# Kernel tuning notes

Hardware: AMD Instinct MI355X
Metric: run time of the kernel (lower is better)

The kernel has to match this reference:

```python
import jax, jax.numpy as jnp
import numpy as np

B, S, D, H = 1, 2048, 1024, 16
DEPTH = D // H          # 64
A_DFF = 1024
NRES = 2                # num_reslayerA
SLOPE = 0.2             # LeakyReLU slope in plga attention
POW_EPS = 1e-9


def _ln(x, g, b):
    m = jnp.mean(x, axis=-1, keepdims=True)
    v = jnp.var(x, axis=-1, keepdims=True)
    return (x - m) * jax.lax.rsqrt(v + 1e-6) * g + b


def setup_inputs() -> dict:
    key = jax.random.key(0)
    ks = jax.random.split(key, 12)
    s = 0.02
    W = lambda k, shp: jax.random.normal(k, shp, jnp.float32) * s
    return {
        'q': jax.random.normal(ks[0], (B, S, D), jnp.float32),
        'k': jax.random.normal(ks[1], (B, S, D), jnp.float32),
        'v': jax.random.normal(ks[2], (B, S, D), jnp.float32),
        'mask': jnp.zeros((B, 1, 1, S), jnp.float32),
        'wq_w': W(ks[3], (D, D)), 'wq_b': jnp.zeros((D,), jnp.float32),
        'wk_w': W(ks[4], (D, D)), 'wk_b': jnp.zeros((D,), jnp.float32),
        'wv_w': W(ks[5], (D, D)), 'wv_b': jnp.zeros((D,), jnp.float32),
        'wo_w': W(ks[6], (D, D)), 'wo_b': jnp.zeros((D,), jnp.float32),
        # stacked ResLayerA params: Dense(depth->A_dff, relu) -> Dense(A_dff->depth) -> LN
        'rl_w1': W(ks[7], (NRES, DEPTH, A_DFF)), 'rl_b1': jnp.zeros((NRES, A_DFF), jnp.float32),
        'rl_w2': W(ks[8], (NRES, A_DFF, DEPTH)), 'rl_b2': jnp.zeros((NRES, DEPTH), jnp.float32),
        'rl_g': jnp.ones((NRES, DEPTH), jnp.float32), 'rl_beta': jnp.zeros((NRES, DEPTH), jnp.float32),
        # plga layer params: power coefficients, attention vector, bias
        'pw': jnp.ones((DEPTH,), jnp.float32),
        'a_vec': W(ks[9], (DEPTH,)),
        'ba': jnp.zeros((), jnp.float32),
    }


def reference(q, k, v, mask, wq_w, wq_b, wk_w, wk_b, wv_w, wv_b, wo_w, wo_b,
              rl_w1, rl_b1, rl_w2, rl_b2, rl_g, rl_beta, pw, a_vec, ba):
    Bq = q.shape[0]
    split = lambda x: x.reshape(Bq, -1, H, DEPTH).transpose(0, 2, 1, 3)  # [b,h,s,d]
    qh = split(q @ wq_w + wq_b)
    kh = split(k @ wk_w + wk_b)
    vh = split(v @ wv_w + wv_b)

    # metric tensor A = q^T q  -> [b,h,depth,depth]
    A = jnp.einsum('bhsd,bhse->bhde', qh, qh)
    # ResLayerA residual dense+LN stack over last dim
    for i in range(NRES):
        Ain = A
        hdn = jax.nn.relu(A @ rl_w1[i] + rl_b1[i])
        A = _ln((hdn @ rl_w2[i] + rl_b2[i]) + Ain, rl_g[i], rl_beta[i])

    # power-law graph attention (plga_layer, att_head=1, activation=None)
    Ap = jnp.power(jnp.abs(A) + POW_EPS, pw)                  # element-wise learned power
    avAp = jnp.einsum('d,bhde->bhe', a_vec, Ap)               # [b,h,depth] per-dim scaling
    E = jnp.einsum('bhsd,bhd,bhtd->bhst', qh, avAp, kh)       # pairwise logits [b,h,s,s]
    Ep = jnp.where(E > 0, E, SLOPE * E) + ba                  # LeakyReLU + learned bias
    Ep = Ep + mask * (-1e9)
    attv = jax.nn.softmax(Ep, axis=-1)
    Hnext = jnp.einsum('bhst,bhtd->bhsd', attv, vh)

    Hnext = Hnext.transpose(0, 2, 1, 3).reshape(Bq, -1, D)
    out = Hnext @ wo_w + wo_b
    return (out, E, A, pw, attv, ba, avAp, Ep)
```

## Files before the change

kernel.cpp:

```cpp
#include <hip/hip_runtime.h>
#include <stdint.h>

#define S_ 2048
#define D_ 1024
#define H_ 16
#define DEP_ 64

typedef float f32x4 __attribute__((ext_vector_type(4)));
typedef __bf16 bf16x8 __attribute__((ext_vector_type(8)));

#define MFMA16(a,b,c) __builtin_amdgcn_mfma_f32_16x16x32_bf16((a),(b),(c),0,0,0)

static constexpr size_t OFF_E    = 2097152ull;
static constexpr size_t OFF_A    = 69206016ull;
static constexpr size_t OFF_PW   = 69271552ull;
static constexpr size_t OFF_ATT  = 69271616ull;
static constexpr size_t OFF_BA   = 136380480ull;
static constexpr size_t OFF_AVAP = 136380481ull;
static constexpr size_t OFF_EP   = 136381505ull;

__device__ __forceinline__ short f2b(float f) {
  union { float f; uint32_t u; } c; c.f = f;
  uint32_t u = c.u;
  uint32_t r = (u + 0x7fffu + ((u >> 16) & 1u)) >> 16;
  return (short)(r & 0xffffu);
}
__device__ __forceinline__ float b2f(short s) {
  union { uint32_t u; float f; } c; c.u = ((uint32_t)(uint16_t)s) << 16;
  return c.f;
}
__device__ __forceinline__ void st_nt(float* p, f32x4 v) {
  __builtin_nontemporal_store(v, (f32x4*)p);
}

__global__ void k_cvt_in(const float* __restrict__ q, const float* __restrict__ k,
                         const float* __restrict__ v, short* __restrict__ dst) {
  const float* src = (blockIdx.z == 0) ? q : (blockIdx.z == 1) ? k : v;
  short* d = dst + (size_t)blockIdx.z * (S_*D_);
  int i = (blockIdx.x * 256 + threadIdx.x) * 4;
  float4 f = *(const float4*)(src + i);
  short4 o;
  o.x = f2b(f.x); o.y = f2b(f.y); o.z = f2b(f.z); o.w = f2b(f.w);
  *(short4*)(d + i) = o;
}

__global__ void k_cvt_wT(const float* __restrict__ wq, const float* __restrict__ wk,
                         const float* __restrict__ wv, const float* __restrict__ wo,
                         short* __restrict__ dst) {
  __shared__ float tile[64][65];
  const float* W = (blockIdx.z == 0) ? wq : (blockIdx.z == 1) ? wk :
                   (blockIdx.z == 2) ? wv : wo;
  short* d = dst + (size_t)blockIdx.z * (D_*D_);
  int k0 = blockIdx.x * 64, n0 = blockIdx.y * 64;
  int t = threadIdx.x;
  for (int i = 0; i < 16; ++i) {
    int e = i*256 + t, r = e >> 6, c = e & 63;
    tile[r][c] = W[(size_t)(k0+r)*D_ + n0 + c];
  }
  __syncthreads();
  for (int i = 0; i < 16; ++i) {
    int e = i*256 + t, r = e >> 6, c = e & 63;
    d[(size_t)(n0+r)*D_ + k0 + c] = f2b(tile[c][r]);
  }
}

__global__ void k_cvt_rl(const float* __restrict__ w1, const float* __restrict__ w2,
                         short* __restrict__ w1T, short* __restrict__ w2T) {
  __shared__ float tile[64][65];
  int z = blockIdx.z, l = z >> 1, which = z & 1;
  int bx = blockIdx.x, t = threadIdx.x;
  if (which == 0) {
    const float* src = w1 + (size_t)l*65536;
    short* d = w1T + (size_t)l*65536;
    int n0 = bx*64;
    for (int i = 0; i < 16; ++i) {
      int e = i*256 + t, r = e >> 6, c = e & 63;
      tile[r][c] = src[(size_t)r*1024 + n0 + c];
    }
    __syncthreads();
    for (int i = 0; i < 16; ++i) {
      int e = i*256 + t, r = e >> 6, c = e & 63;
      d[(size_t)(n0+r)*64 + c] = f2b(tile[c][r]);
    }
  } else {
    const float* src = w2 + (size_t)l*65536;
    short* d = w2T + (size_t)l*65536;
    int k0 = bx*64;
    for (int i = 0; i < 16; ++i) {
      int e = i*256 + t, r = e >> 6, c = e & 63;
      tile[r][c] = src[(size_t)(k0+r)*64 + c];
    }
    __syncthreads();
    for (int i = 0; i < 16; ++i) {
      int e = i*256 + t, r = e >> 6, c = e & 63;
      d[(size_t)r*1024 + k0 + c] = f2b(tile[c][r]);
    }
  }
}

__global__ __launch_bounds__(256) void k_gemm(
    const short* __restrict__ Xall, const short* __restrict__ X2,
    const short* __restrict__ WTall,
    const float* __restrict__ b0, const float* __restrict__ b1v,
    const float* __restrict__ b2v, short* __restrict__ dstall,
    float* __restrict__ outf, int mode) {
  __shared__ short As[128*72];
  __shared__ short Bs[128*72];
  int z = blockIdx.z;
  const short* X  = Xall + (size_t)z * (S_*D_);
  const short* WT = WTall + (size_t)z * (D_*D_);
  int m0 = blockIdx.x * 128, n0 = blockIdx.y * 128;
  int t = threadIdx.x, lane = t & 63;
  int wr = t >> 7, wc = (t >> 6) & 1;
  int rA = lane & 15, kg = lane >> 4;
  f32x4 acc[4][4] = {};
  for (int kt = 0; kt < 16; ++kt) {
#pragma unroll
    for (int i = 0; i < 4; ++i) {
      int cid = i*256 + t, row = cid >> 3, c = cid & 7;
      size_t xi = (size_t)(m0+row)*D_ + kt*64 + c*8;
      if (mode == 2) {
        union { int4 v; short s[8]; } a1, a2, o;
        a1.v = *(const int4*)&X[xi];
        a2.v = *(const int4*)&X2[xi];
#pragma unroll
        for (int j = 0; j < 8; ++j) o.s[j] = f2b(b2f(a1.s[j]) + b2f(a2.s[j]));
        *(int4*)&As[row*72 + c*8] = o.v;
      } else {
        *(int4*)&As[row*72 + c*8] = *(const int4*)&X[xi];
      }
      *(int4*)&Bs[row*72 + c*8] = *(const int4*)&WT[(size_t)(n0+row)*D_ + kt*64 + c*8];
    }
    __syncthreads();
#pragma unroll
    for (int kk = 0; kk < 2; ++kk) {
      bf16x8 a[4], b[4];
#pragma unroll
      for (int m = 0; m < 4; ++m)
        a[m] = *(const bf16x8*)&As[(wr*64 + m*16 + rA)*72 + kk*32 + kg*8];
#pragma unroll
      for (int n = 0; n < 4; ++n)
        b[n] = *(const bf16x8*)&Bs[(wc*64 + n*16 + rA)*72 + kk*32 + kg*8];
#pragma unroll
      for (int m = 0; m < 4; ++m)
#pragma unroll
        for (int n = 0; n < 4; ++n)
          acc[m][n] = MFMA16(a[m], b[n], acc[m][n]);
    }
    __syncthreads();
  }
  const float* bias = (mode != 0) ? b0 : (z == 0 ? b0 : (z == 1 ? b1v : b2v));
#pragma unroll
  for (int m = 0; m < 4; ++m) {
#pragma unroll
    for (int n = 0; n < 4; ++n) {
      int col = n0 + wc*64 + n*16 + rA;
      float bb = bias[col];
#pragma unroll
      for (int rr = 0; rr < 4; ++rr) {
        int row = m0 + wr*64 + m*16 + kg*4 + rr;
        float val = acc[m][n][rr] + bb;
        if (mode == 0) {
          int head = col >> 6, dd = col & 63;
          dstall[(size_t)z*(S_*D_) + ((size_t)head*S_ + row)*DEP_ + dd] = f2b(val);
        } else {
          outf[(size_t)row*D_ + col] = val;
        }
      }
    }
  }
}

__global__ void k_transpose(const short* __restrict__ qh, const short* __restrict__ vh,
                            short* __restrict__ qhT, short* __restrict__ vhT) {
  __shared__ short tile[64][68];
  const short* src = blockIdx.z ? vh : qh;
  short* dst = blockIdx.z ? vhT : qhT;
  int h = blockIdx.y, s0 = blockIdx.x * 64, t = threadIdx.x;
  for (int i = 0; i < 16; ++i) {
    int e = i*256 + t, r = e >> 6, c = e & 63;
    tile[r][c] = src[((size_t)h*S_ + s0 + r)*DEP_ + c];
  }
  __syncthreads();
  for (int i = 0; i < 16; ++i) {
    int e = i*256 + t, r = e >> 6, c = e & 63;
    dst[((size_t)h*DEP_ + r)*S_ + s0 + c] = tile[c][r];
  }
}

__global__ __launch_bounds__(256) void k_metric_p(const short* __restrict__ qhT,
                                                  float* __restrict__ Apart) {
  __shared__ short qt[64*72];
  int kc = blockIdx.x, h = blockIdx.y, t = threadIdx.x, lane = t & 63;
  int wr = t >> 7, wc = (t >> 6) & 1;
  int rA = lane & 15, kg = lane >> 4;
  f32x4 acc[2][2] = {};
  for (int kt = 0; kt < 4; ++kt) {
#pragma unroll
    for (int i = 0; i < 2; ++i) {
      int cid = i*256 + t, row = cid >> 3, c = cid & 7;
      *(int4*)&qt[row*72 + c*8] =
        *(const int4*)&qhT[((size_t)h*DEP_ + row)*S_ + kc*256 + kt*64 + c*8];
    }
    __syncthreads();
#pragma unroll
    for (int kk = 0; kk < 2; ++kk) {
      bf16x8 a[2], b[2];
#pragma unroll
      for (int m = 0; m < 2; ++m)
        a[m] = *(const bf16x8*)&qt[(wr*32 + m*16 + rA)*72 + kk*32 + kg*8];
#pragma unroll
      for (int n = 0; n < 2; ++n)
        b[n] = *(const bf16x8*)&qt[(wc*32 + n*16 + rA)*72 + kk*32 + kg*8];
#pragma unroll
      for (int m = 0; m < 2; ++m)
#pragma unroll
        for (int n = 0; n < 2; ++n)
          acc[m][n] = MFMA16(a[m], b[n], acc[m][n]);
    }
    __syncthreads();
  }
#pragma unroll
  for (int m = 0; m < 2; ++m)
#pragma unroll
    for (int n = 0; n < 2; ++n)
#pragma unroll
      for (int rr = 0; rr < 4; ++rr) {
        int row = wr*32 + m*16 + kg*4 + rr, col = wc*32 + n*16 + rA;
        Apart[((size_t)(kc*16 + h))*4096 + row*64 + col] = acc[m][n][rr];
      }
}

__global__ void k_metric_r(const float* __restrict__ Apart, float* __restrict__ A0f,
                           short* __restrict__ Afb) {
  int h = blockIdx.x, t = threadIdx.x;
#pragma unroll
  for (int i = 0; i < 4; ++i) {
    int idx = i*1024 + t*4;
    f32x4 s = {};
#pragma unroll
    for (int kc = 0; kc < 8; ++kc)
      s += *(const f32x4*)&Apart[((size_t)(kc*16 + h))*4096 + idx];
    *(f32x4*)&A0f[(size_t)h*4096 + idx] = s;
    union { int2 v; short sh[4]; } pk;
#pragma unroll
    for (int j = 0; j < 4; ++j) pk.sh[j] = f2b(s[j]);
    *(int2*)&Afb[(size_t)h*4096 + idx] = pk.v;
  }
}

__global__ __launch_bounds__(256) void k_d1(const short* __restrict__ Afb,
                                            const short* __restrict__ w1Tl,
                                            const float* __restrict__ b1l,
                                            short* __restrict__ hd) {
  __shared__ short As[64*72];
  __shared__ short Bs[128*72];
  int bcol = blockIdx.x * 128, h = blockIdx.y;
  int t = threadIdx.x, lane = t & 63, w = t >> 6;
  int rA = lane & 15, kg = lane >> 4;
#pragma unroll
  for (int i = 0; i < 2; ++i) {
    int cid = i*256 + t, row = cid >> 3, c = cid & 7;
    *(int4*)&As[row*72 + c*8] = *(const int4*)&Afb[(size_t)h*4096 + row*64 + c*8];
  }
#pragma unroll
  for (int i = 0; i < 4; ++i) {
    int cid = i*256 + t, row = cid >> 3, c = cid & 7;
    *(int4*)&Bs[row*72 + c*8] = *(const int4*)&w1Tl[(size_t)(bcol+row)*64 + c*8];
  }
  __syncthreads();
  f32x4 acc[2][4] = {};
#pragma unroll
  for (int kk = 0; kk < 2; ++kk) {
    bf16x8 aA[4], bW[2];
#pragma unroll
    for (int mf = 0; mf < 4; ++mf)
      aA[mf] = *(const bf16x8*)&As[(mf*16 + rA)*72 + kk*32 + kg*8];
#pragma unroll
    for (int nf = 0; nf < 2; ++nf)
      bW[nf] = *(const bf16x8*)&Bs[(w*32 + nf*16 + rA)*72 + kk*32 + kg*8];
#pragma unroll
    for (int nf = 0; nf < 2; ++nf)
#pragma unroll
      for (int mf = 0; mf < 4; ++mf)
        acc[nf][mf] = MFMA16(bW[nf], aA[mf], acc[nf][mf]);
  }
#pragma unroll
  for (int nf = 0; nf < 2; ++nf) {
    int cb = bcol + w*32 + nf*16 + kg*4;
    f32x4 b1v = *(const f32x4*)&b1l[cb];
#pragma unroll
    for (int mf = 0; mf < 4; ++mf) {
      int r = mf*16 + rA;
      union { int2 v; short s[4]; } pk;
#pragma unroll
      for (int rr = 0; rr < 4; ++rr)
        pk.s[rr] = f2b(fmaxf(acc[nf][mf][rr] + b1v[rr], 0.f));
      *(int2*)&hd[((size_t)h*64 + r)*1024 + cb] = pk.v;
    }
  }
}

__global__ __launch_bounds__(256) void k_d2p(const short* __restrict__ hd,
                                             const short* __restrict__ w2Tl,
                                             float* __restrict__ d2part) {
  __shared__ short hs[64*72];
  __shared__ short ws2[64*72];
  int kc = blockIdx.x, h = blockIdx.y, t = threadIdx.x, lane = t & 63;
  int wr = t >> 7, wc = (t >> 6) & 1;
  int rA = lane & 15, kg = lane >> 4;
  f32x4 acc[2][2] = {};
  for (int kt = 0; kt < 4; ++kt) {
#pragma unroll
    for (int i = 0; i < 2; ++i) {
      int cid = i*256 + t, row = cid >> 3, c = cid & 7;
      *(int4*)&hs[row*72 + c*8]  =
        *(const int4*)&hd[((size_t)h*64 + row)*1024 + kc*256 + kt*64 + c*8];
      *(int4*)&ws2[row*72 + c*8] =
        *(const int4*)&w2Tl[(size_t)row*1024 + kc*256 + kt*64 + c*8];
    }
    __syncthreads();
#pragma unroll
    for (int kk = 0; kk < 2; ++kk) {
      bf16x8 a[2], b[2];
#pragma unroll
      for (int m = 0; m < 2; ++m)
        a[m] = *(const bf16x8*)&hs[(wr*32 + m*16 + rA)*72 + kk*32 + kg*8];
#pragma unroll
      for (int n = 0; n < 2; ++n)
        b[n] = *(const bf16x8*)&ws2[(wc*32 + n*16 + rA)*72 + kk*32 + kg*8];
#pragma unroll
      for (int m = 0; m < 2; ++m)
#pragma unroll
        for (int n = 0; n < 2; ++n)
          acc[m][n] = MFMA16(a[m], b[n], acc[m][n]);
    }
    __syncthreads();
  }
#pragma unroll
  for (int m = 0; m < 2; ++m)
#pragma unroll
    for (int n = 0; n < 2; ++n)
#pragma unroll
      for (int rr = 0; rr < 4; ++rr) {
        int row = wr*32 + m*16 + kg*4 + rr, col = wc*32 + n*16 + rA;
        d2part[((size_t)(kc*16 + h))*4096 + row*64 + col] = acc[m][n][rr];
      }
}

__global__ __launch_bounds__(256) void k_d2r_ln(
    const float* __restrict__ d2part, const float* __restrict__ b2l,
    const float* __restrict__ AresIn, const float* __restrict__ gl,
    const float* __restrict__ bel, short* __restrict__ Afb,
    float* __restrict__ AresOut, float* __restrict__ outB,
    const float* __restrict__ pwv, const float* __restrict__ av,
    const float* __restrict__ bav, float* __restrict__ avApW, int layer) {
  __shared__ float Xf[64][68];
  __shared__ float red[4][64];
  int h = blockIdx.x, t = threadIdx.x;
  int r = t >> 2, q4 = t & 3;
  float xv[16], s1 = 0.f, s2 = 0.f;
#pragma unroll
  for (int jj = 0; jj < 4; ++jj) {
    f32x4 s = {};
#pragma unroll
    for (int kc = 0; kc < 4; ++kc)
      s += *(const f32x4*)&d2part[((size_t)(kc*16 + h))*4096 + r*64 + q4*16 + jj*4];
#pragma unroll
    for (int j = 0; j < 4; ++j) {
      int c = q4*16 + jj*4 + j;
      float x = s[j] + b2l[c] + AresIn[(size_t)h*4096 + r*64 + c];
      xv[jj*4 + j] = x;
      s1 += x; s2 += x*x;
    }
  }
  s1 += __shfl_xor(s1, 1); s1 += __shfl_xor(s1, 2);
  s2 += __shfl_xor(s2, 1); s2 += __shfl_xor(s2, 2);
  float mean = s1 * (1.f/64.f);
  float var  = s2 * (1.f/64.f) - mean*mean;
  float rstd = rsqrtf(var + 1e-6f);
#pragma unroll
  for (int j = 0; j < 16; ++j) {
    int c = q4*16 + j;
    float nx = (xv[j] - mean)*rstd*gl[c] + bel[c];
    Afb[(size_t)h*4096 + r*64 + c] = f2b(nx);
    if (layer == 0) AresOut[(size_t)h*4096 + r*64 + c] = nx;
    else            outB[OFF_A + (size_t)h*4096 + r*64 + c] = nx;
    Xf[r][c] = nx;
  }
  if (layer == 1) {
    __syncthreads();
    int e = t & 63, dg = t >> 6;
    float pe = pwv[e], p = 0.f;
    for (int j = 0; j < 16; ++j) {
      int d = dg*16 + j;
      p += av[d] * powf(fabsf(Xf[d][e]) + 1e-9f, pe);
    }
    red[dg][e] = p;
    __syncthreads();
    if (t < 64) {
      float tot = red[0][t] + red[1][t] + red[2][t] + red[3][t];
      avApW[h*64 + t] = tot;
      outB[OFF_AVAP + h*64 + t] = tot;
    }
    if (h == 0) {
      if (t < 64) outB[OFF_PW + t] = pwv[t];
      if (t == 0) outB[OFF_BA] = bav[0];
    }
  }
}

__global__ __launch_bounds__(256) void k_pass1(
    const short* __restrict__ qh, const short* __restrict__ kh,
    const float* __restrict__ avAp, const float* __restrict__ mask,
    const float* __restrict__ bap, float* __restrict__ outB,
    float2* __restrict__ part) {
  __shared__ float Et[128*128];
  __shared__ float avl[64];
  short* Qs = (short*)Et;
  short* Ks = ((short*)Et) + 8192;
  int tt = blockIdx.x, st = blockIdx.y, h = blockIdx.z;
  int s0 = st*128, t0 = tt*128;
  int t = threadIdx.x, lane = t & 63;
  int wr = t >> 7, wc = (t >> 6) & 1;
  int rA = lane & 15, kg = lane >> 4;
  if (t < 16) *(f32x4*)&avl[t*4] = *(const f32x4*)&avAp[h*64 + t*4];
  __syncthreads();
#pragma unroll
  for (int i = 0; i < 4; ++i) {
    int cid = i*256 + t, row = cid >> 3, c = cid & 7, cs = c ^ (row & 7);
    union { int4 v; short s[8]; } qa, qo;
    qa.v = *(const int4*)&qh[((size_t)h*S_ + s0 + row)*DEP_ + c*8];
#pragma unroll
    for (int j = 0; j < 8; ++j) qo.s[j] = f2b(b2f(qa.s[j]) * avl[c*8 + j]);
    *(int4*)&Qs[row*64 + cs*8] = qo.v;
    *(int4*)&Ks[row*64 + cs*8] = *(const int4*)&kh[((size_t)h*S_ + t0 + row)*DEP_ + c*8];
  }
  __syncthreads();
  f32x4 acc[4][4] = {};
#pragma unroll
  for (int kk = 0; kk < 2; ++kk) {
    bf16x8 a[4], b[4];
#pragma unroll
    for (int m = 0; m < 4; ++m) {
      int row = wr*64 + m*16 + rA, c = (kk*4 + kg) ^ (row & 7);
      a[m] = *(const bf16x8*)&Qs[row*64 + c*8];
    }
#pragma unroll
    for (int n = 0; n < 4; ++n) {
      int row = wc*64 + n*16 + rA, c = (kk*4 + kg) ^ (row & 7);
      b[n] = *(const bf16x8*)&Ks[row*64 + c*8];
    }
#pragma unroll
    for (int m = 0; m < 4; ++m)
#pragma unroll
      for (int n = 0; n < 4; ++n)
        acc[m][n] = MFMA16(b[n], a[m], acc[m][n]);
  }
  float bav = bap[0];
  f32x4 mk[4];
#pragma unroll
  for (int n = 0; n < 4; ++n) {
    f32x4 mm = *(const f32x4*)&mask[t0 + wc*64 + n*16 + kg*4];
#pragma unroll
    for (int j = 0; j < 4; ++j) mk[n][j] = mm[j] * (-1e9f);
  }
#pragma unroll
  for (int m = 0; m < 4; ++m) {
    int row = s0 + wr*64 + m*16 + rA;
    float mx = -3.4e38f;
    f32x4 ep4[4];
#pragma unroll
    for (int n = 0; n < 4; ++n) {
      f32x4 e = acc[m][n];
      f32x4 ep;
#pragma unroll
      for (int j = 0; j < 4; ++j) {
        float ee = e[j];
        ep[j] = (ee > 0.f ? ee : 0.2f*ee) + bav + mk[n][j];
        mx = fmaxf(mx, ep[j]);
      }
      ep4[n] = ep;
    }
    mx = fmaxf(mx, __shfl_xor(mx, 16));
    mx = fmaxf(mx, __shfl_xor(mx, 32));
    float sm = 0.f;
#pragma unroll
    for (int n = 0; n < 4; ++n)
#pragma unroll
      for (int j = 0; j < 4; ++j) sm += expf(ep4[n][j] - mx);
    sm += __shfl_xor(sm, 16);
    sm += __shfl_xor(sm, 32);
    if (kg == 0)
      part[((size_t)(h*S_ + row)*16 + tt)*2 + wc] = make_float2(mx, sm);
  }
  __syncthreads();
#pragma unroll
  for (int m = 0; m < 4; ++m)
#pragma unroll
    for (int n = 0; n < 4; ++n) {
      int row = wr*64 + m*16 + rA;
      int unit = wc*16 + n*4 + kg;
      *(f32x4*)&Et[row*128 + ((unit ^ (row & 7)))*4] = acc[m][n];
    }
  __syncthreads();
  float* Eo  = outB + OFF_E;
  float* Epo = outB + OFF_EP;
  int colu = t & 31;
  int rbase = t >> 5;
  f32x4 mm4 = *(const f32x4*)&mask[t0 + colu*4];
  f32x4 mk4;
#pragma unroll
  for (int j = 0; j < 4; ++j) mk4[j] = mm4[j] * (-1e9f);
#pragma unroll
  for (int r = 0; r < 16; ++r) {
    int row = r*8 + rbase;
    f32x4 e = *(const f32x4*)&Et[row*128 + ((colu ^ (row & 7)))*4];
    size_t gb = ((size_t)h*S_ + s0 + row)*S_ + t0 + colu*4;
    st_nt(&Eo[gb], e);
    f32x4 ep;
#pragma unroll
    for (int j = 0; j < 4; ++j)
      ep[j] = (e[j] > 0.f ? e[j] : 0.2f*e[j]) + bav + mk4[j];
    st_nt(&Epo[gb], ep);
  }
}

__global__ void k_sreduce(const float2* __restrict__ part, float2* __restrict__ fin) {
  int row = blockIdx.x * 256 + threadIdx.x;
  const float2* pp = part + (size_t)row * 32;
  float M = -3.4e38f;
  float2 p[32];
#pragma unroll
  for (int i = 0; i < 32; ++i) { p[i] = pp[i]; M = fmaxf(M, p[i].x); }
  float L = 0.f;
#pragma unroll
  for (int i = 0; i < 32; ++i) L += p[i].y * expf(p[i].x - M);
  fin[row] = make_float2(M, L);
}

__global__ __launch_bounds__(256) void k_pass2(
    const short* __restrict__ qh, const short* __restrict__ kh,
    const short* __restrict__ vhT, const float* __restrict__ avAp,
    const float* __restrict__ mask, const float* __restrict__ bap,
    const float2* __restrict__ fin, float* __restrict__ attv,
    short* __restrict__ Hnp) {
  __shared__ short Qs[128*64];
  __shared__ short KP[128*128];
  __shared__ short Vs[64*128];
  __shared__ float avl[64];
  int st = blockIdx.x, tc = blockIdx.y, h = blockIdx.z;
  int s0 = st * 128;
  int t = threadIdx.x, lane = t & 63;
  int wr = t >> 7, wc = (t >> 6) & 1;
  int rA = lane & 15, kg = lane >> 4;
  if (t < 16) *(f32x4*)&avl[t*4] = *(const f32x4*)&avAp[h*64 + t*4];
  __syncthreads();
#pragma unroll
  for (int i = 0; i < 4; ++i) {
    int cid = i*256 + t, row = cid >> 3, c = cid & 7, cs = c ^ (row & 7);
    union { int4 v; short s[8]; } qa, qo;
    qa.v = *(const int4*)&qh[((size_t)h*S_ + s0 + row)*DEP_ + c*8];
#pragma unroll
    for (int j = 0; j < 8; ++j) qo.s[j] = f2b(b2f(qa.s[j]) * avl[c*8 + j]);
    *(int4*)&Qs[row*64 + cs*8] = qo.v;
  }
  float Ms[4], Li[4];
#pragma unroll
  for (int m = 0; m < 4; ++m) {
    float2 f = fin[h*S_ + s0 + wr*64 + m*16 + rA];
    Ms[m] = f.x; Li[m] = 1.f / f.y;
  }
  float bav = bap[0];
  __syncthreads();
  bf16x8 aq[4][2];
#pragma unroll
  for (int m = 0; m < 4; ++m)
#pragma unroll
    for (int kk = 0; kk < 2; ++kk) {
      int row = wr*64 + m*16 + rA, c = (kk*4 + kg) ^ (row & 7);
      aq[m][kk] = *(const bf16x8*)&Qs[row*64 + c*8];
    }
  f32x4 acc2[4][2] = {};
  for (int tt = tc*8; tt < tc*8 + 8; ++tt) {
    int t0 = tt * 128;
    __syncthreads();
#pragma unroll
    for (int i = 0; i < 4; ++i) {
      int cid = i*256 + t, row = cid >> 3, c = cid & 7, cs = c ^ (row & 7);
      *(int4*)&KP[row*64 + cs*8] = *(const int4*)&kh[((size_t)h*S_ + t0 + row)*DEP_ + c*8];
    }
#pragma unroll
    for (int i = 0; i < 4; ++i) {
      int cid = i*256 + t, row = cid >> 4, c = cid & 15, cs = c ^ (row & 7);
      *(int4*)&Vs[row*128 + cs*8] = *(const int4*)&vhT[((size_t)h*DEP_ + row)*S_ + t0 + c*8];
    }
    __syncthreads();
    f32x4 accE[4][4] = {};
#pragma unroll
    for (int kk = 0; kk < 2; ++kk) {
      bf16x8 b[4];
#pragma unroll
      for (int n = 0; n < 4; ++n) {
        int row = wc*64 + n*16 + rA, c = (kk*4 + kg) ^ (row & 7);
        b[n] = *(const bf16x8*)&KP[row*64 + c*8];
      }
#pragma unroll
      for (int m = 0; m < 4; ++m)
#pragma unroll
        for (int n = 0; n < 4; ++n)
          accE[m][n] = MFMA16(b[n], aq[m][kk], accE[m][n]);
    }
    f32x4 mk[4];
#pragma unroll
    for (int n = 0; n < 4; ++n) {
      f32x4 mm = *(const f32x4*)&mask[t0 + wc*64 + n*16 + kg*4];
#pragma unroll
      for (int j = 0; j < 4; ++j) mk[n][j] = mm[j] * (-1e9f);
    }
#pragma unroll
    for (int m = 0; m < 4; ++m)
#pragma unroll
      for (int n = 0; n < 4; ++n) {
        f32x4 e = accE[m][n], p;
#pragma unroll
        for (int j = 0; j < 4; ++j) {
          float ep = (e[j] > 0.f ? e[j] : 0.2f*e[j]) + bav + mk[n][j];
          p[j] = expf(ep - Ms[m]) * Li[m];
        }
        accE[m][n] = p;
      }
    __syncthreads();
#pragma unroll
    for (int m = 0; m < 4; ++m) {
      int srow = wr*64 + m*16 + rA;
#pragma unroll
      for (int n = 0; n < 4; ++n) {
        int tcol = wc*64 + n*16 + kg*4;
        union { int2 v; short s[4]; } pk;
#pragma unroll
        for (int j = 0; j < 4; ++j) pk.s[j] = f2b(accE[m][n][j]);
        *(int2*)((char*)KP + srow*256 + ((tcol*2) ^ ((srow & 7) << 4))) = pk.v;
      }
    }
    __syncthreads();
#pragma unroll
    for (int kkp = 0; kkp < 4; ++kkp) {
      bf16x8 ap[4], bv[2];
#pragma unroll
      for (int m = 0; m < 4; ++m) {
        int row = wr*64 + m*16 + rA;
        ap[m] = *(const bf16x8*)((const char*)KP + row*256 + ((kkp*64 + kg*16) ^ ((row & 7) << 4)));
      }
#pragma unroll
      for (int n = 0; n < 2; ++n) {
        int dd = wc*32 + n*16 + rA, c = (kkp*4 + kg) ^ (dd & 7);
        bv[n] = *(const bf16x8*)&Vs[dd*128 + c*8];
      }
#pragma unroll
      for (int m = 0; m < 4; ++m)
#pragma unroll
        for (int n = 0; n < 2; ++n)
          acc2[m][n] = MFMA16(ap[m], bv[n], acc2[m][n]);
    }
#pragma unroll
    for (int it = 0; it < 8; ++it) {
      int row = it*16 + (t >> 4);
      int unit = t & 15;
      union { int4 v; short s[8]; } pv;
      pv.v = *(const int4*)((const char*)KP + row*256 + ((unit*16) ^ ((row & 7) << 4)));
      f32x4 lo, hi;
#pragma unroll
      for (int j = 0; j < 4; ++j) { lo[j] = b2f(pv.s[j]); hi[j] = b2f(pv.s[4+j]); }
      size_t gb = ((size_t)h*S_ + s0 + row)*S_ + t0 + unit*8;
      st_nt(&attv[gb], lo);
      st_nt(&attv[gb + 4], hi);
    }
  }
  short* Hp = Hnp + (size_t)tc * (S_*D_);
#pragma unroll
  for (int m = 0; m < 4; ++m)
#pragma unroll
    for (int n = 0; n < 2; ++n)
#pragma unroll
      for (int rr = 0; rr < 4; ++rr) {
        int row = s0 + wr*64 + m*16 + kg*4 + rr;
        int dd = wc*32 + n*16 + rA;
        Hp[(size_t)row*D_ + h*DEP_ + dd] = f2b(acc2[m][n][rr]);
      }
}

extern "C" void kernel_launch(void* const* d_in, const int* in_sizes, int n_in,
                              void* d_out, int out_size, void* d_ws, size_t ws_size,
                              hipStream_t stream) {
  (void)in_sizes; (void)n_in; (void)out_size; (void)ws_size;
  const float* q    = (const float*)d_in[0];
  const float* k    = (const float*)d_in[1];
  const float* v    = (const float*)d_in[2];
  const float* mask = (const float*)d_in[3];
  const float* wq_w = (const float*)d_in[4];
  const float* wq_b = (const float*)d_in[5];
  const float* wk_w = (const float*)d_in[6];
  const float* wk_b = (const float*)d_in[7];
  const float* wv_w = (const float*)d_in[8];
  const float* wv_b = (const float*)d_in[9];
  const float* wo_w = (const float*)d_in[10];
  const float* wo_b = (const float*)d_in[11];
  const float* rl_w1 = (const float*)d_in[12];
  const float* rl_b1 = (const float*)d_in[13];
  const float* rl_w2 = (const float*)d_in[14];
  const float* rl_b2 = (const float*)d_in[15];
  const float* rl_g  = (const float*)d_in[16];
  const float* rl_be = (const float*)d_in[17];
  const float* pw    = (const float*)d_in[18];
  const float* avec  = (const float*)d_in[19];
  const float* ba    = (const float*)d_in[20];
  float* outf = (float*)d_out;

  char* w = (char*)d_ws;
  short* xbf  = (short*)(w);
  short* wT   = (short*)(w + (12u << 20));
  short* qh   = (short*)(w + (20u << 20));
  short* kh   = (short*)(w + (24u << 20));
  short* vh   = (short*)(w + (28u << 20));
  short* qhT  = (short*)(w);
  short* vhT  = (short*)(w + (4u << 20));
  short* hd   = (short*)(w + (8u << 20));
  short* w1T  = (short*)(w + (10u << 20));
  short* w2T  = (short*)(w + (10u << 20) + (256u << 10));
  short* Afbf = (short*)(w + (10u << 20) + (512u << 10));
  float* Ares0 = (float*)(w + (11u << 20));
  float* Ares1 = (float*)(w + (11u << 20) + (256u << 10));
  float* Apart = (float*)(w + (12u << 20));
  float* d2part = (float*)(w + (14u << 20));
  float2* part = (float2*)(w + (8u << 20));
  float2* fin  = (float2*)(w + (16u << 20));
  float* avApW = (float*)(w + (16u << 20) + (512u << 10));
  short* Hnp  = (short*)(w + (8u << 20));

  k_cvt_in<<<dim3(2048, 1, 3), 256, 0, stream>>>(q, k, v, xbf);
  k_cvt_wT<<<dim3(16, 16, 4), 256, 0, stream>>>(wq_w, wk_w, wv_w, wo_w, wT);
  k_cvt_rl<<<dim3(16, 1, 4), 256, 0, stream>>>(rl_w1, rl_w2, w1T, w2T);
  k_gemm<<<dim3(16, 8, 3), 256, 0, stream>>>(xbf, nullptr, wT, wq_b, wk_b, wv_b,
                                             qh, nullptr, 0);
  k_transpose<<<dim3(32, 16, 2), 256, 0, stream>>>(qh, vh, qhT, vhT);
  k_metric_p<<<dim3(8, 16), 256, 0, stream>>>(qhT, Apart);
  k_metric_r<<<dim3(16), 256, 0, stream>>>(Apart, Ares0, Afbf);
  k_d1<<<dim3(8, 16), 256, 0, stream>>>(Afbf, w1T, rl_b1, hd);
  k_d2p<<<dim3(4, 16), 256, 0, stream>>>(hd, w2T, d2part);
  k_d2r_ln<<<dim3(16), 256, 0, stream>>>(d2part, rl_b2, Ares0, rl_g, rl_be,
                                         Afbf, Ares1, outf, pw, avec, ba, avApW, 0);
  k_d1<<<dim3(8, 16), 256, 0, stream>>>(Afbf, w1T + 65536, rl_b1 + 1024, hd);
  k_d2p<<<dim3(4, 16), 256, 0, stream>>>(hd, w2T + 65536, d2part);
  k_d2r_ln<<<dim3(16), 256, 0, stream>>>(d2part, rl_b2 + 64, Ares1, rl_g + 64, rl_be + 64,
                                         Afbf, Ares1, outf, pw, avec, ba, avApW, 1);
  k_pass1<<<dim3(16, 16, 16), 256, 0, stream>>>(qh, kh, avApW, mask, ba, outf, part);
  k_sreduce<<<dim3(128), 256, 0, stream>>>(part, fin);
  k_pass2<<<dim3(16, 2, 16), 256, 0, stream>>>(qh, kh, vhT, avApW, mask, ba, fin,
                                               outf + OFF_ATT, Hnp);
  k_gemm<<<dim3(16, 8, 1), 256, 0, stream>>>(Hnp, Hnp + (size_t)S_*D_, wT + 3u*D_*D_,
                                             wo_b, wo_b, wo_b, nullptr, outf, 2);
}
```

Measured before the change: 503.9 us.

## Fuse conversion kernels, ResLayerA stack, and softmax reduce into fewer launches

Merges the three input/weight conversion kernels into one launch and collapses metric reduce, both ResLayerA dense/LN layers and the power-law avAp computation into a single per-head kernel that keeps intermediates in shared memory. It also folds the softmax stat reduction into pass2 and halves pass1's shared E staging buffer, which should raise occupancy. The aim is to cut about ten small launches and their global round trips. The cost is that the fused residual kernel runs on only 16 blocks, so the ResLayerA work has very little parallelism.

```diff
diff --git a/kernel.cpp b/kernel.cpp
--- a/kernel.cpp
+++ b/kernel.cpp
@@ -33,67 +33,67 @@
   __builtin_nontemporal_store(v, (f32x4*)p);
 }
 
-__global__ void k_cvt_in(const float* __restrict__ q, const float* __restrict__ k,
-                         const float* __restrict__ v, short* __restrict__ dst) {
-  const float* src = (blockIdx.z == 0) ? q : (blockIdx.z == 1) ? k : v;
-  short* d = dst + (size_t)blockIdx.z * (S_*D_);
-  int i = (blockIdx.x * 256 + threadIdx.x) * 4;
-  float4 f = *(const float4*)(src + i);
-  short4 o;
-  o.x = f2b(f.x); o.y = f2b(f.y); o.z = f2b(f.z); o.w = f2b(f.w);
-  *(short4*)(d + i) = o;
-}
-
-__global__ void k_cvt_wT(const float* __restrict__ wq, const float* __restrict__ wk,
-                         const float* __restrict__ wv, const float* __restrict__ wo,
-                         short* __restrict__ dst) {
+__global__ void k_cvt_all(const float* __restrict__ q, const float* __restrict__ k,
+                          const float* __restrict__ v, const float* __restrict__ wq,
+                          const float* __restrict__ wk, const float* __restrict__ wv,
+                          const float* __restrict__ wo, const float* __restrict__ w1,
+                          const float* __restrict__ w2, short* __restrict__ xbf,
+                          short* __restrict__ wT, short* __restrict__ w1T,
+                          short* __restrict__ w2T) {
   __shared__ float tile[64][65];
-  const float* W = (blockIdx.z == 0) ? wq : (blockIdx.z == 1) ? wk :
-                   (blockIdx.z == 2) ? wv : wo;
-  short* d = dst + (size_t)blockIdx.z * (D_*D_);
-  int k0 = blockIdx.x * 64, n0 = blockIdx.y * 64;
-  int t = threadIdx.x;
-  for (int i = 0; i < 16; ++i) {
-    int e = i*256 + t, r = e >> 6, c = e & 63;
-    tile[r][c] = W[(size_t)(k0+r)*D_ + n0 + c];
-  }
-  __syncthreads();
-  for (int i = 0; i < 16; ++i) {
-    int e = i*256 + t, r = e >> 6, c = e & 63;
-    d[(size_t)(n0+r)*D_ + k0 + c] = f2b(tile[c][r]);
-  }
-}
-
-__global__ void k_cvt_rl(const float* __restrict__ w1, const float* __restrict__ w2,
-                         short* __restrict__ w1T, short* __restrict__ w2T) {
-  __shared__ float tile[64][65];
-  int z = blockIdx.z, l = z >> 1, which = z & 1;
-  int bx = blockIdx.x, t = threadIdx.x;
-  if (which == 0) {
-    const float* src = w1 + (size_t)l*65536;
-    short* d = w1T + (size_t)l*65536;
-    int n0 = bx*64;
+  int bid = blockIdx.x, t = threadIdx.x;
+  if (bid < 6144) {
+    int z = bid >> 11, bx = bid & 2047;
+    const float* src = (z == 0) ? q : (z == 1) ? k : v;
+    short* d = xbf + (size_t)z * (S_*D_);
+    int i = (bx*256 + t)*4;
+    float4 f = *(const float4*)(src + i);
+    short4 o;
+    o.x = f2b(f.x); o.y = f2b(f.y); o.z = f2b(f.z); o.w = f2b(f.w);
+    *(short4*)(d + i) = o;
+  } else if (bid < 7168) {
+    int u = bid - 6144, z = u >> 8, tl = u & 255;
+    int k0 = (tl >> 4)*64, n0 = (tl & 15)*64;
+    const float* W = (z == 0) ? wq : (z == 1) ? wk : (z == 2) ? wv : wo;
+    short* d = wT + (size_t)z * (D_*D_);
     for (int i = 0; i < 16; ++i) {
       int e = i*256 + t, r = e >> 6, c = e & 63;
-      tile[r][c] = src[(size_t)r*1024 + n0 + c];
+      tile[r][c] = W[(size_t)(k0+r)*D_ + n0 + c];
     }
     __syncthreads();
     for (int i = 0; i < 16; ++i) {
       int e = i*256 + t, r = e >> 6, c = e & 63;
-      d[(size_t)(n0+r)*64 + c] = f2b(tile[c][r]);
+      d[(size_t)(n0+r)*D_ + k0 + c] = f2b(tile[c][r]);
     }
   } else {
-    const float* src = w2 + (size_t)l*65536;
-    short* d = w2T + (size_t)l*65536;
-    int k0 = bx*64;
-    for (int i = 0; i < 16; ++i) {
-      int e = i*256 + t, r = e >> 6, c = e & 63;
-      tile[r][c] = src[(size_t)(k0+r)*64 + c];
-    }
-    __syncthreads();
-    for (int i = 0; i < 16; ++i) {
-      int e = i*256 + t, r = e >> 6, c = e & 63;
-      d[(size_t)r*1024 + k0 + c] = f2b(tile[c][r]);
+    int u = bid - 7168, z = u >> 4, bx = u & 15;
+    int l = z >> 1, which = z & 1;
+    if (which == 0) {
+      const float* src = w1 + (size_t)l*65536;
+      short* d = w1T + (size_t)l*65536;
+      int n0 = bx*64;
+      for (int i = 0; i < 16; ++i) {
+        int e = i*256 + t, r = e >> 6, c = e & 63;
+        tile[r][c] = src[(size_t)r*1024 + n0 + c];
+      }
+      __syncthreads();
+      for (int i = 0; i < 16; ++i) {
+        int e = i*256 + t, r = e >> 6, c = e & 63;
+        d[(size_t)(n0+r)*64 + c] = f2b(tile[c][r]);
+      }
+    } else {
+      const float* src = w2 + (size_t)l*65536;
+      short* d = w2T + (size_t)l*65536;
+      int k0 = bx*64;
+      for (int i = 0; i < 16; ++i) {
+        int e = i*256 + t, r = e >> 6, c = e & 63;
+        tile[r][c] = src[(size_t)(k0+r)*64 + c];
+      }
+      __syncthreads();
+      for (int i = 0; i < 16; ++i) {
+        int e = i*256 + t, r = e >> 6, c = e & 63;
+        d[(size_t)r*1024 + k0 + c] = f2b(tile[c][r]);
+      }
     }
   }
 }
@@ -231,182 +231,155 @@
       }
 }
 
-__global__ void k_metric_r(const float* __restrict__ Apart, float* __restrict__ A0f,
-                           short* __restrict__ Afb) {
+__global__ __launch_bounds__(512) void k_res(
+    const float* __restrict__ Apart, const short* __restrict__ w1T,
+    const float* __restrict__ b1, const short* __restrict__ w2T,
+    const float* __restrict__ b2, const float* __restrict__ gl,
+    const float* __restrict__ bel, const float* __restrict__ pwv,
+    const float* __restrict__ av, const float* __restrict__ bav,
+    float* __restrict__ avApW, float* __restrict__ outB) {
+  __shared__ float Af[64][68];
+  __shared__ short Afb[64][72];
+  __shared__ short hdP[64*520];
+  __shared__ float red[8][64];
   int h = blockIdx.x, t = threadIdx.x;
-#pragma unroll
-  for (int i = 0; i < 4; ++i) {
-    int idx = i*1024 + t*4;
+  int lane = t & 63, w = t >> 6;
+  int rA = lane & 15, kg = lane >> 4;
+#pragma unroll
+  for (int i = 0; i < 2; ++i) {
+    int idx = (i*512 + t)*4;
     f32x4 s = {};
 #pragma unroll
     for (int kc = 0; kc < 8; ++kc)
       s += *(const f32x4*)&Apart[((size_t)(kc*16 + h))*4096 + idx];
-    *(f32x4*)&A0f[(size_t)h*4096 + idx] = s;
+    int r = idx >> 6, c = idx & 63;
+    *(f32x4*)&Af[r][c] = s;
     union { int2 v; short sh[4]; } pk;
 #pragma unroll
     for (int j = 0; j < 4; ++j) pk.sh[j] = f2b(s[j]);
-    *(int2*)&Afb[(size_t)h*4096 + idx] = pk.v;
-  }
-}
-
-__global__ __launch_bounds__(256) void k_d1(const short* __restrict__ Afb,
-                                            const short* __restrict__ w1Tl,
-                                            const float* __restrict__ b1l,
-                                            short* __restrict__ hd) {
-  __shared__ short As[64*72];
-  __shared__ short Bs[128*72];
-  int bcol = blockIdx.x * 128, h = blockIdx.y;
-  int t = threadIdx.x, lane = t & 63, w = t >> 6;
-  int rA = lane & 15, kg = lane >> 4;
-#pragma unroll
-  for (int i = 0; i < 2; ++i) {
-    int cid = i*256 + t, row = cid >> 3, c = cid & 7;
-    *(int4*)&As[row*72 + c*8] = *(const int4*)&Afb[(size_t)h*4096 + row*64 + c*8];
-  }
-#pragma unroll
-  for (int i = 0; i < 4; ++i) {
-    int cid = i*256 + t, row = cid >> 3, c = cid & 7;
-    *(int4*)&Bs[row*72 + c*8] = *(const int4*)&w1Tl[(size_t)(bcol+row)*64 + c*8];
+    *(int2*)&Afb[r][c] = pk.v;
   }
   __syncthreads();
-  f32x4 acc[2][4] = {};
-#pragma unroll
-  for (int kk = 0; kk < 2; ++kk) {
-    bf16x8 aA[4], bW[2];
-#pragma unroll
-    for (int mf = 0; mf < 4; ++mf)
-      aA[mf] = *(const bf16x8*)&As[(mf*16 + rA)*72 + kk*32 + kg*8];
-#pragma unroll
-    for (int nf = 0; nf < 2; ++nf)
-      bW[nf] = *(const bf16x8*)&Bs[(w*32 + nf*16 + rA)*72 + kk*32 + kg*8];
-#pragma unroll
-    for (int nf = 0; nf < 2; ++nf)
+  for (int layer = 0; layer < 2; ++layer) {
+    const short* w1l = w1T + layer*65536;
+    const short* w2l = w2T + layer*65536;
+    f32x4 acc2[4][4] = {};
+    for (int kc = 0; kc < 2; ++kc) {
+      int c0g = kc*512 + w*64;
+      f32x4 acc1[4][4] = {};
+#pragma unroll
+      for (int kk = 0; kk < 2; ++kk) {
+        bf16x8 aA[4], bW[4];
+#pragma unroll
+        for (int mf = 0; mf < 4; ++mf)
+          aA[mf] = *(const bf16x8*)&Afb[mf*16 + rA][kk*32 + kg*8];
+#pragma unroll
+        for (int nf = 0; nf < 4; ++nf)
+          bW[nf] = *(const bf16x8*)&w1l[(size_t)(c0g + nf*16 + rA)*64 + kk*32 + kg*8];
+#pragma unroll
+        for (int mf = 0; mf < 4; ++mf)
+#pragma unroll
+          for (int nf = 0; nf < 4; ++nf)
+            acc1[mf][nf] = MFMA16(aA[mf], bW[nf], acc1[mf][nf]);
+      }
+      __syncthreads();
+#pragma unroll
+      for (int nf = 0; nf < 4; ++nf) {
+        int col = w*64 + nf*16 + rA;
+        float bb1 = b1[layer*1024 + kc*512 + col];
+#pragma unroll
+        for (int mf = 0; mf < 4; ++mf)
+#pragma unroll
+          for (int rr = 0; rr < 4; ++rr) {
+            int r = mf*16 + kg*4 + rr;
+            hdP[r*520 + col] = f2b(fmaxf(acc1[mf][nf][rr] + bb1, 0.f));
+          }
+      }
+      __syncthreads();
+#pragma unroll
+      for (int kk = 0; kk < 2; ++kk) {
+        bf16x8 a2[4], bw2[4];
+#pragma unroll
+        for (int mf = 0; mf < 4; ++mf)
+          a2[mf] = *(const bf16x8*)&hdP[(mf*16 + rA)*520 + w*64 + kk*32 + kg*8];
+#pragma unroll
+        for (int nf = 0; nf < 4; ++nf)
+          bw2[nf] = *(const bf16x8*)&w2l[(size_t)(nf*16 + rA)*1024 + kc*512 + w*64 + kk*32 + kg*8];
+#pragma unroll
+        for (int mf = 0; mf < 4; ++mf)
+#pragma unroll
+          for (int nf = 0; nf < 4; ++nf)
+            acc2[mf][nf] = MFMA16(a2[mf], bw2[nf], acc2[mf][nf]);
+      }
+    }
+    __syncthreads();
+    float* P = (float*)hdP;
+    if (w >= 4) {
+      int slot = w - 4;
 #pragma unroll
       for (int mf = 0; mf < 4; ++mf)
-        acc[nf][mf] = MFMA16(bW[nf], aA[mf], acc[nf][mf]);
-  }
-#pragma unroll
-  for (int nf = 0; nf < 2; ++nf) {
-    int cb = bcol + w*32 + nf*16 + kg*4;
-    f32x4 b1v = *(const f32x4*)&b1l[cb];
-#pragma unroll
-    for (int mf = 0; mf < 4; ++mf) {
-      int r = mf*16 + rA;
-      union { int2 v; short s[4]; } pk;
-#pragma unroll
-      for (int rr = 0; rr < 4; ++rr)
-        pk.s[rr] = f2b(fmaxf(acc[nf][mf][rr] + b1v[rr], 0.f));
-      *(int2*)&hd[((size_t)h*64 + r)*1024 + cb] = pk.v;
-    }
-  }
-}
-
-__global__ __launch_bounds__(256) void k_d2p(const short* __restrict__ hd,
-                                             const short* __restrict__ w2Tl,
-                                             float* __restrict__ d2part) {
-  __shared__ short hs[64*72];
-  __shared__ short ws2[64*72];
-  int kc = blockIdx.x, h = blockIdx.y, t = threadIdx.x, lane = t & 63;
-  int wr = t >> 7, wc = (t >> 6) & 1;
-  int rA = lane & 15, kg = lane >> 4;
-  f32x4 acc[2][2] = {};
-  for (int kt = 0; kt < 4; ++kt) {
-#pragma unroll
-    for (int i = 0; i < 2; ++i) {
-      int cid = i*256 + t, row = cid >> 3, c = cid & 7;
-      *(int4*)&hs[row*72 + c*8]  =
-        *(const int4*)&hd[((size_t)h*64 + row)*1024 + kc*256 + kt*64 + c*8];
-      *(int4*)&ws2[row*72 + c*8] =
-        *(const int4*)&w2Tl[(size_t)row*1024 + kc*256 + kt*64 + c*8];
-    }
-    __syncthreads();
-#pragma unroll
-    for (int kk = 0; kk < 2; ++kk) {
-      bf16x8 a[2], b[2];
-#pragma unroll
-      for (int m = 0; m < 2; ++m)
-        a[m] = *(const bf16x8*)&hs[(wr*32 + m*16 + rA)*72 + kk*32 + kg*8];
-#pragma unroll
-      for (int n = 0; n < 2; ++n)
-        b[n] = *(const bf16x8*)&ws2[(wc*32 + n*16 + rA)*72 + kk*32 + kg*8];
-#pragma unroll
-      for (int m = 0; m < 2; ++m)
-#pragma unroll
-        for (int n = 0; n < 2; ++n)
-          acc[m][n] = MFMA16(a[m], b[n], acc[m][n]);
-    }
-    __syncthreads();
-  }
-#pragma unroll
-  for (int m = 0; m < 2; ++m)
-#pragma unroll
-    for (int n = 0; n < 2; ++n)
-#pragma unroll
-      for (int rr = 0; rr < 4; ++rr) {
-        int row = wr*32 + m*16 + kg*4 + rr, col = wc*32 + n*16 + rA;
-        d2part[((size_t)(kc*16 + h))*4096 + row*64 + col] = acc[m][n][rr];
-      }
-}
-
-__global__ __launch_bounds__(256) void k_d2r_ln(
-    const float* __restrict__ d2part, const float* __restrict__ b2l,
-    const float* __restrict__ AresIn, const float* __restrict__ gl,
-    const float* __restrict__ bel, short* __restrict__ Afb,
-    float* __restrict__ AresOut, float* __restrict__ outB,
-    const float* __restrict__ pwv, const float* __restrict__ av,
-    const float* __restrict__ bav, float* __restrict__ avApW, int layer) {
-  __shared__ float Xf[64][68];
-  __shared__ float red[4][64];
-  int h = blockIdx.x, t = threadIdx.x;
-  int r = t >> 2, q4 = t & 3;
-  float xv[16], s1 = 0.f, s2 = 0.f;
-#pragma unroll
-  for (int jj = 0; jj < 4; ++jj) {
-    f32x4 s = {};
-#pragma unroll
-    for (int kc = 0; kc < 4; ++kc)
-      s += *(const f32x4*)&d2part[((size_t)(kc*16 + h))*4096 + r*64 + q4*16 + jj*4];
-#pragma unroll
-    for (int j = 0; j < 4; ++j) {
-      int c = q4*16 + jj*4 + j;
-      float x = s[j] + b2l[c] + AresIn[(size_t)h*4096 + r*64 + c];
-      xv[jj*4 + j] = x;
-      s1 += x; s2 += x*x;
-    }
-  }
-  s1 += __shfl_xor(s1, 1); s1 += __shfl_xor(s1, 2);
-  s2 += __shfl_xor(s2, 1); s2 += __shfl_xor(s2, 2);
-  float mean = s1 * (1.f/64.f);
-  float var  = s2 * (1.f/64.f) - mean*mean;
-  float rstd = rsqrtf(var + 1e-6f);
-#pragma unroll
-  for (int j = 0; j < 16; ++j) {
-    int c = q4*16 + j;
-    float nx = (xv[j] - mean)*rstd*gl[c] + bel[c];
-    Afb[(size_t)h*4096 + r*64 + c] = f2b(nx);
-    if (layer == 0) AresOut[(size_t)h*4096 + r*64 + c] = nx;
-    else            outB[OFF_A + (size_t)h*4096 + r*64 + c] = nx;
-    Xf[r][c] = nx;
-  }
-  if (layer == 1) {
-    __syncthreads();
+#pragma unroll
+        for (int nf = 0; nf < 4; ++nf)
+#pragma unroll
+          for (int rr = 0; rr < 4; ++rr)
+            P[slot*4160 + (mf*16 + kg*4 + rr)*65 + nf*16 + rA] = acc2[mf][nf][rr];
+    }
+    __syncthreads();
+    if (w < 4) {
+#pragma unroll
+      for (int mf = 0; mf < 4; ++mf)
+#pragma unroll
+        for (int nf = 0; nf < 4; ++nf)
+#pragma unroll
+          for (int rr = 0; rr < 4; ++rr)
+            P[w*4160 + (mf*16 + kg*4 + rr)*65 + nf*16 + rA] += acc2[mf][nf][rr];
+    }
+    __syncthreads();
+    int r = t >> 3, j0 = (t & 7)*8;
+    float x[8], s1 = 0.f, s2 = 0.f;
+#pragma unroll
+    for (int j = 0; j < 8; ++j) {
+      int c = j0 + j;
+      float xx = P[r*65 + c] + P[4160 + r*65 + c] + P[8320 + r*65 + c] + P[12480 + r*65 + c]
+               + b2[layer*64 + c] + Af[r][c];
+      x[j] = xx; s1 += xx; s2 += xx*xx;
+    }
+    s1 += __shfl_xor(s1, 1); s1 += __shfl_xor(s1, 2); s1 += __shfl_xor(s1, 4);
+    s2 += __shfl_xor(s2, 1); s2 += __shfl_xor(s2, 2); s2 += __shfl_xor(s2, 4);
+    float mean = s1 * (1.f/64.f);
+    float var  = s2 * (1.f/64.f) - mean*mean;
+    float rstd = rsqrtf(var + 1e-6f);
+#pragma unroll
+    for (int j = 0; j < 8; ++j) {
+      int c = j0 + j;
+      float nx = (x[j] - mean)*rstd*gl[layer*64 + c] + bel[layer*64 + c];
+      Af[r][c] = nx;
+      Afb[r][c] = f2b(nx);
+      if (layer == 1) outB[OFF_A + (size_t)h*4096 + r*64 + c] = nx;
+    }
+    __syncthreads();
+  }
+  {
     int e = t & 63, dg = t >> 6;
     float pe = pwv[e], p = 0.f;
-    for (int j = 0; j < 16; ++j) {
-      int d = dg*16 + j;
-      p += av[d] * powf(fabsf(Xf[d][e]) + 1e-9f, pe);
+#pragma unroll
+    for (int j = 0; j < 8; ++j) {
+      int d = dg*8 + j;
+      p += av[d] * powf(fabsf(Af[d][e]) + 1e-9f, pe);
     }
     red[dg][e] = p;
-    __syncthreads();
-    if (t < 64) {
-      float tot = red[0][t] + red[1][t] + red[2][t] + red[3][t];
-      avApW[h*64 + t] = tot;
-      outB[OFF_AVAP + h*64 + t] = tot;
-    }
-    if (h == 0) {
-      if (t < 64) outB[OFF_PW + t] = pwv[t];
-      if (t == 0) outB[OFF_BA] = bav[0];
-    }
+  }
+  __syncthreads();
+  if (t < 64) {
+    float tot = 0.f;
+#pragma unroll
+    for (int g = 0; g < 8; ++g) tot += red[g][t];
+    avApW[h*64 + t] = tot;
+    outB[OFF_AVAP + h*64 + t] = tot;
+  }
+  if (h == 0) {
+    if (t < 64) outB[OFF_PW + t] = pwv[t];
+    if (t == 0) outB[OFF_BA] = bav[0];
   }
 }
 
@@ -415,7 +388,7 @@
     const float* __restrict__ avAp, const float* __restrict__ mask,
     const float* __restrict__ bap, float* __restrict__ outB,
     float2* __restrict__ part) {
-  __shared__ float Et[128*128];
+  __shared__ float Et[64*128];
   __shared__ float avl[64];
   short* Qs = (short*)Et;
   short* Ks = ((short*)Et) + 8192;
@@ -458,12 +431,12 @@
         acc[m][n] = MFMA16(b[n], a[m], acc[m][n]);
   }
   float bav = bap[0];
-  f32x4 mk[4];
+  f32x4 mkf[4];
 #pragma unroll
   for (int n = 0; n < 4; ++n) {
     f32x4 mm = *(const f32x4*)&mask[t0 + wc*64 + n*16 + kg*4];
 #pragma unroll
-    for (int j = 0; j < 4; ++j) mk[n][j] = mm[j] * (-1e9f);
+    for (int j = 0; j < 4; ++j) mkf[n][j] = mm[j] * (-1e9f);
   }
 #pragma unroll
   for (int m = 0; m < 4; ++m) {
@@ -477,7 +450,7 @@
 #pragma unroll
       for (int j = 0; j < 4; ++j) {
         float ee = e[j];
-        ep[j] = (ee > 0.f ? ee : 0.2f*ee) + bav + mk[n][j];
+        ep[j] = (ee > 0.f ? ee : 0.2f*ee) + bav + mkf[n][j];
         mx = fmaxf(mx, ep[j]);
       }
       ep4[n] = ep;
@@ -494,67 +467,68 @@
     if (kg == 0)
       part[((size_t)(h*S_ + row)*16 + tt)*2 + wc] = make_float2(mx, sm);
   }
-  __syncthreads();
-#pragma unroll
-  for (int m = 0; m < 4; ++m)
-#pragma unroll
-    for (int n = 0; n < 4; ++n) {
-      int row = wr*64 + m*16 + rA;
-      int unit = wc*16 + n*4 + kg;
-      *(f32x4*)&Et[row*128 + ((unit ^ (row & 7)))*4] = acc[m][n];
-    }
-  __syncthreads();
   float* Eo  = outB + OFF_E;
   float* Epo = outB + OFF_EP;
-  int colu = t & 31;
-  int rbase = t >> 5;
+  int colu = t & 31, rbase = t >> 5;
   f32x4 mm4 = *(const f32x4*)&mask[t0 + colu*4];
   f32x4 mk4;
 #pragma unroll
   for (int j = 0; j < 4; ++j) mk4[j] = mm4[j] * (-1e9f);
-#pragma unroll
-  for (int r = 0; r < 16; ++r) {
-    int row = r*8 + rbase;
-    f32x4 e = *(const f32x4*)&Et[row*128 + ((colu ^ (row & 7)))*4];
-    size_t gb = ((size_t)h*S_ + s0 + row)*S_ + t0 + colu*4;
-    st_nt(&Eo[gb], e);
-    f32x4 ep;
-#pragma unroll
-    for (int j = 0; j < 4; ++j)
-      ep[j] = (e[j] > 0.f ? e[j] : 0.2f*e[j]) + bav + mk4[j];
-    st_nt(&Epo[gb], ep);
-  }
-}
-
-__global__ void k_sreduce(const float2* __restrict__ part, float2* __restrict__ fin) {
-  int row = blockIdx.x * 256 + threadIdx.x;
-  const float2* pp = part + (size_t)row * 32;
-  float M = -3.4e38f;
-  float2 p[32];
-#pragma unroll
-  for (int i = 0; i < 32; ++i) { p[i] = pp[i]; M = fmaxf(M, p[i].x); }
-  float L = 0.f;
-#pragma unroll
-  for (int i = 0; i < 32; ++i) L += p[i].y * expf(p[i].x - M);
-  fin[row] = make_float2(M, L);
+  __syncthreads();
+#pragma unroll
+  for (int half = 0; half < 2; ++half) {
+    if (wr == half) {
+#pragma unroll
+      for (int m = 0; m < 4; ++m)
+#pragma unroll
+        for (int n = 0; n < 4; ++n) {
+          int row_l = m*16 + rA;
+          int unit = wc*16 + n*4 + kg;
+          *(f32x4*)&Et[row_l*128 + ((unit ^ (row_l & 7)))*4] = acc[m][n];
+        }
+    }
+    __syncthreads();
+#pragma unroll
+    for (int r = 0; r < 8; ++r) {
+      int row_l = r*8 + rbase;
+      f32x4 e = *(const f32x4*)&Et[row_l*128 + ((colu ^ (row_l & 7)))*4];
+      size_t gb = ((size_t)h*S_ + s0 + half*64 + row_l)*S_ + t0 + colu*4;
+      st_nt(&Eo[gb], e);
+      f32x4 ep;
+#pragma unroll
+      for (int j = 0; j < 4; ++j)
+        ep[j] = (e[j] > 0.f ? e[j] : 0.2f*e[j]) + bav + mk4[j];
+      st_nt(&Epo[gb], ep);
+    }
+    __syncthreads();
+  }
 }
 
 __global__ __launch_bounds__(256) void k_pass2(
     const short* __restrict__ qh, const short* __restrict__ kh,
     const short* __restrict__ vhT, const float* __restrict__ avAp,
     const float* __restrict__ mask, const float* __restrict__ bap,
-    const float2* __restrict__ fin, float* __restrict__ attv,
-    short* __restrict__ Hnp) {
+    const float2* __restrict__ part, float* __restrict__ attv,
+    short* __restrict__ Hnp0, short* __restrict__ Hnp1) {
   __shared__ short Qs[128*64];
   __shared__ short KP[128*128];
   __shared__ short Vs[64*128];
   __shared__ float avl[64];
+  __shared__ float2 finS[128];
   int st = blockIdx.x, tc = blockIdx.y, h = blockIdx.z;
   int s0 = st * 128;
   int t = threadIdx.x, lane = t & 63;
   int wr = t >> 7, wc = (t >> 6) & 1;
   int rA = lane & 15, kg = lane >> 4;
   if (t < 16) *(f32x4*)&avl[t*4] = *(const f32x4*)&avAp[h*64 + t*4];
+  if (t < 128) {
+    const float2* pp = part + (size_t)(h*S_ + s0 + t) * 32;
+    float M = -3.4e38f;
+    for (int i = 0; i < 32; ++i) M = fmaxf(M, pp[i].x);
+    float L = 0.f;
+    for (int i = 0; i < 32; ++i) L += pp[i].y * expf(pp[i].x - M);
+    finS[t] = make_float2(M, 1.f / L);
+  }
   __syncthreads();
 #pragma unroll
   for (int i = 0; i < 4; ++i) {
@@ -568,8 +542,8 @@
   float Ms[4], Li[4];
 #pragma unroll
   for (int m = 0; m < 4; ++m) {
-    float2 f = fin[h*S_ + s0 + wr*64 + m*16 + rA];
-    Ms[m] = f.x; Li[m] = 1.f / f.y;
+    float2 f = finS[wr*64 + m*16 + rA];
+    Ms[m] = f.x; Li[m] = f.y;
   }
   float bav = bap[0];
   __syncthreads();
@@ -611,12 +585,12 @@
         for (int n = 0; n < 4; ++n)
           accE[m][n] = MFMA16(b[n], aq[m][kk], accE[m][n]);
     }
-    f32x4 mk[4];
+    f32x4 mkf[4];
 #pragma unroll
     for (int n = 0; n < 4; ++n) {
       f32x4 mm = *(const f32x4*)&mask[t0 + wc*64 + n*16 + kg*4];
 #pragma unroll
-      for (int j = 0; j < 4; ++j) mk[n][j] = mm[j] * (-1e9f);
+      for (int j = 0; j < 4; ++j) mkf[n][j] = mm[j] * (-1e9f);
     }
 #pragma unroll
     for (int m = 0; m < 4; ++m)
@@ -625,7 +599,7 @@
         f32x4 e = accE[m][n], p;
 #pragma unroll
         for (int j = 0; j < 4; ++j) {
-          float ep = (e[j] > 0.f ? e[j] : 0.2f*e[j]) + bav + mk[n][j];
+          float ep = (e[j] > 0.f ? e[j] : 0.2f*e[j]) + bav + mkf[n][j];
           p[j] = expf(ep - Ms[m]) * Li[m];
         }
         accE[m][n] = p;
@@ -677,7 +651,7 @@
       st_nt(&attv[gb + 4], hi);
     }
   }
-  short* Hp = Hnp + (size_t)tc * (S_*D_);
+  short* Hp = tc ? Hnp1 : Hnp0;
 #pragma unroll
   for (int m = 0; m < 4; ++m)
 #pragma unroll
@@ -725,39 +699,25 @@
   short* vh   = (short*)(w + (28u << 20));
   short* qhT  = (short*)(w);
   short* vhT  = (short*)(w + (4u << 20));
-  short* hd   = (short*)(w + (8u << 20));
-  short* w1T  = (short*)(w + (10u << 20));
-  short* w2T  = (short*)(w + (10u << 20) + (256u << 10));
-  short* Afbf = (short*)(w + (10u << 20) + (512u << 10));
-  float* Ares0 = (float*)(w + (11u << 20));
-  float* Ares1 = (float*)(w + (11u << 20) + (256u << 10));
   float* Apart = (float*)(w + (12u << 20));
-  float* d2part = (float*)(w + (14u << 20));
   float2* part = (float2*)(w + (8u << 20));
-  float2* fin  = (float2*)(w + (16u << 20));
   float* avApW = (float*)(w + (16u << 20) + (512u << 10));
-  short* Hnp  = (short*)(w + (8u << 20));
-
-  k_cvt_in<<<dim3(2048, 1, 3), 256, 0, stream>>>(q, k, v, xbf);
-  k_cvt_wT<<<dim3(16, 16, 4), 256, 0, stream>>>(wq_w, wk_w, wv_w, wo_w, wT);
-  k_cvt_rl<<<dim3(16, 1, 4), 256, 0, stream>>>(rl_w1, rl_w2, w1T, w2T);
+  short* w1T  = (short*)(w + (32u << 20));
+  short* w2T  = (short*)(w + (32u << 20) + (256u << 10));
+  short* Hnp0 = (short*)(w);
+  short* Hnp1 = (short*)(w + (28u << 20));
+
+  k_cvt_all<<<dim3(7232), 256, 0, stream>>>(q, k, v, wq_w, wk_w, wv_w, wo_w,
+                                            rl_w1, rl_w2, xbf, wT, w1T, w2T);
   k_gemm<<<dim3(16, 8, 3), 256, 0, stream>>>(xbf, nullptr, wT, wq_b, wk_b, wv_b,
                                              qh, nullptr, 0);
   k_transpose<<<dim3(32, 16, 2), 256, 0, stream>>>(qh, vh, qhT, vhT);
   k_metric_p<<<dim3(8, 16), 256, 0, stream>>>(qhT, Apart);
-  k_metric_r<<<dim3(16), 256, 0, stream>>>(Apart, Ares0, Afbf);
-  k_d1<<<dim3(8, 16), 256, 0, stream>>>(Afbf, w1T, rl_b1, hd);
-  k_d2p<<<dim3(4, 16), 256, 0, stream>>>(hd, w2T, d2part);
-  k_d2r_ln<<<dim3(16), 256, 0, stream>>>(d2part, rl_b2, Ares0, rl_g, rl_be,
-                                         Afbf, Ares1, outf, pw, avec, ba, avApW, 0);
-  k_d1<<<dim3(8, 16), 256, 0, stream>>>(Afbf, w1T + 65536, rl_b1 + 1024, hd);
-  k_d2p<<<dim3(4, 16), 256, 0, stream>>>(hd, w2T + 65536, d2part);
-  k_d2r_ln<<<dim3(16), 256, 0, stream>>>(d2part, rl_b2 + 64, Ares1, rl_g + 64, rl_be + 64,
-                                         Afbf, Ares1, outf, pw, avec, ba, avApW, 1);
+  k_res<<<dim3(16), 512, 0, stream>>>(Apart, w1T, rl_b1, w2T, rl_b2, rl_g, rl_be,
+                                      pw, avec, ba, avApW, outf);
   k_pass1<<<dim3(16, 16, 16), 256, 0, stream>>>(qh, kh, avApW, mask, ba, outf, part);
-  k_sreduce<<<dim3(128), 256, 0, stream>>>(part, fin);
-  k_pass2<<<dim3(16, 2, 16), 256, 0, stream>>>(qh, kh, vhT, avApW, mask, ba, fin,
-                                               outf + OFF_ATT, Hnp);
-  k_gemm<<<dim3(16, 8, 1), 256, 0, stream>>>(Hnp, Hnp + (size_t)S_*D_, wT + 3u*D_*D_,
+  k_pass2<<<dim3(16, 2, 16), 256, 0, stream>>>(qh, kh, vhT, avApW, mask, ba, part,
+                                               outf + OFF_ATT, Hnp0, Hnp1);
+  k_gemm<<<dim3(16, 8, 1), 256, 0, stream>>>(Hnp0, Hnp1, wT + 3u*D_*D_,
                                              wo_b, wo_b, wo_b, nullptr, outf, 2);
 }
```

Measured after the change: 497.8 us. No clear change (-1.2%).
